# Optimization experiments

Measured on AMD Instinct MI355X. Metric: run time of the kernel, lower is better.

The kernel has to match this reference:

```python
import jax, jax.numpy as jnp
import numpy as np
from jax import lax

B, L = 4, 1024
D_MODEL, D_STATE, D_CONV = 512, 16, 4
D_INNER = 2 * D_MODEL          # expand=2
DT_RANK = D_MODEL // 16        # ceil(512/16)=32
K_EXPERTS = 2                  # num_experts_per_token; only first k experts are used
EPS = 1e-5


def setup_inputs() -> dict:
    key = jax.random.key(0)
    ks = jax.random.split(key, 14)
    def n(k, shape, scale=0.02):
        return jax.random.normal(k, shape, jnp.float32) * scale
    # Mamba S4D-real init for A: A_log = log(1..d_state) broadcast over channels
    A_log = jnp.log(jnp.broadcast_to(jnp.arange(1, D_STATE + 1, dtype=jnp.float32), (D_INNER, D_STATE)))
    return {
        "x": jax.random.normal(ks[0], (B, L, D_MODEL), jnp.float32),
        "in_proj_w": n(ks[1], (2 * D_INNER, D_MODEL)),
        "conv_w": n(ks[2], (D_INNER, 1, D_CONV), 0.1),
        "conv_b": n(ks[3], (D_INNER,), 0.1),
        "x_proj_w": n(ks[4], (DT_RANK + 2 * D_STATE, D_INNER)),
        "dt_proj_w": n(ks[5], (D_INNER, DT_RANK), 0.1),
        "dt_proj_b": n(ks[6], (D_INNER,), 0.1),
        "A_log": A_log,
        "D_skip": jnp.ones((D_INNER,), jnp.float32),
        "out_proj_w": n(ks[7], (D_MODEL, D_INNER)),
        "moe_w1": n(ks[8], (K_EXPERTS, 2 * D_MODEL, D_MODEL)),
        "moe_b1": n(ks[9], (K_EXPERTS, 2 * D_MODEL)),
        "moe_w2": n(ks[10], (K_EXPERTS, D_MODEL, 2 * D_MODEL)),
        "moe_b2": n(ks[11], (K_EXPERTS, D_MODEL)),
    }


def _layernorm(x):
    # fresh nn.LayerNorm each forward: weight=1, bias=0, eps=1e-5
    mu = jnp.mean(x, -1, keepdims=True)
    var = jnp.mean(jnp.square(x - mu), -1, keepdims=True)
    return (x - mu) / jnp.sqrt(var + EPS)


def _mamba(x, in_proj_w, conv_w, conv_b, x_proj_w, dt_proj_w, dt_proj_b, A_log, D_skip, out_proj_w):
    b = x.shape[0]
    xz = x @ in_proj_w.T                               # (b, L, 2*d_inner)
    xc, z = jnp.split(xz, 2, axis=-1)
    # causal depthwise conv1d (torch pads both sides with d_conv-1 then slices [:L])
    conv = lax.conv_general_dilated(
        xc.transpose(0, 2, 1), conv_w, (1,), [(D_CONV - 1, 0)],
        feature_group_count=D_INNER) + conv_b[None, :, None]
    xs = jax.nn.silu(conv).transpose(0, 2, 1)          # (b, L, d_inner)
    dbc = xs @ x_proj_w.T                              # (b, L, dt_rank + 2*d_state)
    dt = dbc[..., :DT_RANK]
    Bm = dbc[..., DT_RANK:DT_RANK + D_STATE]           # (b, L, d_state)
    Cm = dbc[..., DT_RANK + D_STATE:]                  # (b, L, d_state)
    delta = jax.nn.softplus(dt @ dt_proj_w.T + dt_proj_b)  # (b, L, d_inner)
    A = -jnp.exp(A_log)                                # (d_inner, d_state)
    dA = jnp.exp(jnp.einsum('bld,dn->bldn', delta, A))     # (b, L, d_inner, d_state)
    dBx = (delta * xs)[..., None] * Bm[:, :, None, :]       # (b, L, d_inner, d_state)

    def step(h, inp):
        dA_t, dBx_t, C_t = inp
        h = dA_t * h + dBx_t                           # (b, d_inner, d_state)
        y = jnp.einsum('bdn,bn->bd', h, C_t)
        return h, y

    h0 = jnp.zeros((b, D_INNER, D_STATE), x.dtype)
    _, ys = lax.scan(step, h0, (dA.transpose(1, 0, 2, 3), dBx.transpose(1, 0, 2, 3), Cm.transpose(1, 0, 2)))
    y = ys.transpose(1, 0, 2) + xs * D_skip            # (b, L, d_inner)
    y = y * jax.nn.silu(z)
    return y @ out_proj_w.T                            # (b, L, d_model)


def reference(x, in_proj_w, conv_w, conv_b, x_proj_w, dt_proj_w, dt_proj_b,
              A_log, D_skip, out_proj_w, moe_w1, moe_b1, moe_w2, moe_b2):
    skip = x
    h = _layernorm(x)
    h = _mamba(h, in_proj_w, conv_w, conv_b, x_proj_w, dt_proj_w, dt_proj_b, A_log, D_skip, out_proj_w) + h
    h = _layernorm(h)
    # static 'MoE': unweighted average of the first K_EXPERTS dense FFNs
    a = jax.nn.relu(jnp.einsum('bld,ekd->belk', h, moe_w1) + moe_b1[None, :, None, :])
    moe = jnp.einsum('belk,edk->beld', a, moe_w2) + moe_b2[None, :, None, :]
    return jnp.mean(moe, axis=1) + skip
```

## Files before the change

### kernel.cpp

```cpp
#include <hip/hip_runtime.h>
#include <hip/hip_bf16.h>

#define BB 4
#define LL 1024
#define DM 512
#define DI 1024
#define DS 16
#define DTR 32
#define MM (BB*LL)

#define ACT_NONE 0
#define ACT_RELU 1

#define CHUNK 128
#define NCH (LL/CHUNK)
#define NSTATE 65536

typedef __attribute__((ext_vector_type(8))) __bf16 bf16x8;
typedef __attribute__((ext_vector_type(8))) unsigned short us8;
typedef __attribute__((ext_vector_type(4))) float f32x4;

__device__ __forceinline__ unsigned short f2bf(float f) {
  union { float f; unsigned int u; } a; a.f = f;
  unsigned int r = a.u + 0x7fffu + ((a.u >> 16) & 1u);
  return (unsigned short)(r >> 16);
}
__device__ __forceinline__ float b2f(unsigned short u) {
  union { unsigned int i; float f; } a; a.i = (unsigned int)u << 16; return a.f;
}

__device__ __forceinline__ bf16x8 ld_frag(const unsigned short* p) {
  us8 s = *(const us8*)p;
  return __builtin_bit_cast(bf16x8, s);
}

__device__ __forceinline__ void gload16(const void* g, void* l) {
  __builtin_amdgcn_global_load_lds(
      (const __attribute__((address_space(1))) void*)g,
      (__attribute__((address_space(3))) void*)l, 16, 0, 0);
}

__global__ __launch_bounds__(256) void prep_ln_kernel(
    const float* __restrict__ x,
    const float* __restrict__ in_proj_w, const float* __restrict__ x_proj_w,
    const float* __restrict__ out_proj_w,
    const float* __restrict__ moe_w1,    const float* __restrict__ moe_w2,
    const float* __restrict__ moe_b2,
    float* __restrict__ h1, unsigned short* __restrict__ h1b,
    unsigned short* __restrict__ inpb,  unsigned short* __restrict__ xpjb,
    unsigned short* __restrict__ outpb,
    unsigned short* __restrict__ w1b,   unsigned short* __restrict__ w2cb,
    float* __restrict__ b2avg)
{
  __shared__ float red[8];
  int bid = blockIdx.x;
  if (bid < MM) {
    int row = bid;
    const float* p = x + (size_t)row * DM;
    float2 v = ((const float2*)p)[threadIdx.x];
    float s  = v.x + v.y;
    float ss = v.x*v.x + v.y*v.y;
    for (int o = 32; o; o >>= 1) { s += __shfl_down(s, o); ss += __shfl_down(ss, o); }
    int wid = threadIdx.x >> 6, lane = threadIdx.x & 63;
    if (lane == 0) { red[wid] = s; red[4+wid] = ss; }
    __syncthreads();
    s  = red[0]+red[1]+red[2]+red[3];
    ss = red[4]+red[5]+red[6]+red[7];
    float mu = s * (1.f/DM);
    float var = ss * (1.f/DM) - mu*mu;
    float rstd = rsqrtf(var + 1e-5f);
    float2 o2; o2.x = (v.x-mu)*rstd; o2.y = (v.y-mu)*rstd;
    ((float2*)(h1 + (size_t)row*DM))[threadIdx.x] = o2;
    ushort2 u; u.x = f2bf(o2.x); u.y = f2bf(o2.y);
    ((ushort2*)(h1b + (size_t)row*DM))[threadIdx.x] = u;
    return;
  }
  int i = (bid - MM) * 256 + threadIdx.x;
  int i4 = i * 4;
  auto cvt4 = [&](const float* src, unsigned short* dst) {
    float4 v = ((const float4*)src)[i];
    ushort4 o; o.x = f2bf(v.x); o.y = f2bf(v.y); o.z = f2bf(v.z); o.w = f2bf(v.w);
    ((ushort4*)dst)[i] = o;
  };
  if (i4 < 2*DI*DM) cvt4(in_proj_w, inpb);
  if (i4 < 64*DI)   cvt4(x_proj_w, xpjb);
  if (i4 < DM*DI)   cvt4(out_proj_w, outpb);
  if (i4 < 2*(2*DM)*DM) cvt4(moe_w1, w1b);
  if (i4 < DM*2*DI) {
    #pragma unroll
    for (int j = 0; j < 4; ++j) {
      int idx = i4 + j;
      int nrow = idx >> 11;
      int t = idx & (2*DI - 1);
      int e = t >> 10;
      int k = t & (DI - 1);
      w2cb[idx] = f2bf(moe_w2[((size_t)e*DM + nrow)*DI + k]);
    }
  }
  if (i4 < DM) {
    #pragma unroll
    for (int j = 0; j < 4; ++j)
      b2avg[i4+j] = 0.5f * (moe_b2[i4+j] + moe_b2[DM + i4+j]);
  }
}

__global__ __launch_bounds__(256) void ln_kernel(const float* __restrict__ in,
                                                 float* __restrict__ outf,
                                                 unsigned short* __restrict__ outb) {
  int row = blockIdx.x;
  const float* p = in + (size_t)row * DM;
  float2 v = ((const float2*)p)[threadIdx.x];
  float s  = v.x + v.y;
  float ss = v.x*v.x + v.y*v.y;
  for (int o = 32; o; o >>= 1) { s += __shfl_down(s, o); ss += __shfl_down(ss, o); }
  __shared__ float red[8];
  int wid = threadIdx.x >> 6, lane = threadIdx.x & 63;
  if (lane == 0) { red[wid] = s; red[4+wid] = ss; }
  __syncthreads();
  s  = red[0]+red[1]+red[2]+red[3];
  ss = red[4]+red[5]+red[6]+red[7];
  float mu = s * (1.f/DM);
  float var = ss * (1.f/DM) - mu*mu;
  float rstd = rsqrtf(var + 1e-5f);
  float2 o2; o2.x = (v.x-mu)*rstd; o2.y = (v.y-mu)*rstd;
  if (outf) ((float2*)(outf + (size_t)row*DM))[threadIdx.x] = o2;
  if (outb) {
    ushort2 u; u.x = f2bf(o2.x); u.y = f2bf(o2.y);
    ((ushort2*)(outb + (size_t)row*DM))[threadIdx.x] = u;
  }
}

template<int BM, int BN, int BK, int WR, int WC, int FM, int FN, int ACT,
         bool OUTF, bool OUTB>
__global__ __launch_bounds__(256) void gemm_mfma(
    const unsigned short* __restrict__ A, int lda,
    const unsigned short* __restrict__ B, int ldb,
    const float* __restrict__ bias,
    const float* __restrict__ res, int ldres,
    float* __restrict__ Cf, unsigned short* __restrict__ Cb, int ldc,
    int K, float scale, int nbx)
{
  static_assert(WR*WC == 4 && WR*FM*16 == BM && WC*FN*16 == BN, "geom");
  constexpr int ATILE = BM*BK, BTILE = BN*BK;
  constexpr int AL = ATILE/2048, BL = BTILE/2048;
  constexpr bool SWZ = (BK == 64);
  __shared__ unsigned short As[2*ATILE];
  __shared__ unsigned short Bs[2*BTILE];
  const int tid = threadIdx.x;
  const int nwg = gridDim.x;
  const int bid = blockIdx.x;
  const int cpx = nwg >> 3;
  const int wid = ((nwg & 7) == 0) ? ((bid & 7)*cpx + (bid >> 3)) : bid;
  const int bm = (wid / nbx) * BM;
  const int bn = (wid % nbx) * BN;
  const int w = tid >> 6, lane = tid & 63;
  const int wr = w / WC, wc = w % WC;
  const int rl = lane & 15, kg = lane >> 4;

  auto stage = [&](int buf, int k0) {
    #pragma unroll
    for (int it = 0; it < AL; ++it) {
      int o = (it*256 + tid) * 16;
      int os = SWZ ? (o ^ (((o>>7)&7)<<4)) : o;
      int e = os >> 1;
      int r = e / BK, c = e % BK;
      gload16(A + (size_t)(bm + r)*lda + k0 + c, (char*)As + buf*ATILE*2 + o);
    }
    #pragma unroll
    for (int it = 0; it < BL; ++it) {
      int o = (it*256 + tid) * 16;
      int os = SWZ ? (o ^ (((o>>7)&7)<<4)) : o;
      int e = os >> 1;
      int r = e / BK, c = e % BK;
      gload16(B + (size_t)(bn + r)*ldb + k0 + c, (char*)Bs + buf*BTILE*2 + o);
    }
  };

  f32x4 acc[FM][FN];
  #pragma unroll
  for (int m = 0; m < FM; ++m)
    #pragma unroll
    for (int n = 0; n < FN; ++n) { f32x4 z = {0.f,0.f,0.f,0.f}; acc[m][n] = z; }

  auto compute = [&](int buf) {
    #pragma unroll
    for (int kk = 0; kk < BK/32; ++kk) {
      bf16x8 af[FM], bfv[FN];
      #pragma unroll
      for (int m = 0; m < FM; ++m) {
        int byte = ((wr*FM*16 + m*16 + rl)*BK + kk*32 + kg*8) * 2;
        if (SWZ) byte ^= ((byte>>7)&7)<<4;
        af[m] = ld_frag((const unsigned short*)((const char*)As + buf*ATILE*2 + byte));
      }
      #pragma unroll
      for (int n = 0; n < FN; ++n) {
        int byte = ((wc*FN*16 + n*16 + rl)*BK + kk*32 + kg*8) * 2;
        if (SWZ) byte ^= ((byte>>7)&7)<<4;
        bfv[n] = ld_frag((const unsigned short*)((const char*)Bs + buf*BTILE*2 + byte));
      }
      #pragma unroll
      for (int m = 0; m < FM; ++m)
        #pragma unroll
        for (int n = 0; n < FN; ++n)
          acc[m][n] = __builtin_amdgcn_mfma_f32_16x16x32_bf16(af[m], bfv[n], acc[m][n], 0, 0, 0);
    }
  };

  stage(0, 0);
  const int nk = K / BK;
  for (int it = 0; it < nk; ++it) {
    if (it + 1 < nk) {
      stage((it&1)^1, (it+1)*BK);
      asm volatile("s_waitcnt vmcnt(%0)" :: "i"(AL+BL) : "memory");
    } else {
      asm volatile("s_waitcnt vmcnt(0)" ::: "memory");
    }
    __builtin_amdgcn_s_barrier();
    compute(it & 1);
    __builtin_amdgcn_s_barrier();
  }

  #pragma unroll
  for (int m = 0; m < FM; ++m) {
    int row = bm + wr*FM*16 + m*16 + kg*4;
    #pragma unroll
    for (int n = 0; n < FN; ++n) {
      int col = bn + wc*FN*16 + n*16 + rl;
      float bv = bias ? bias[col] : 0.f;
      #pragma unroll
      for (int j = 0; j < 4; ++j) {
        float v = acc[m][n][j] * scale + bv;
        if (ACT == ACT_RELU) v = fmaxf(v, 0.f);
        if (res) v += res[(size_t)(row + j)*ldres + col];
        size_t off = (size_t)(row + j)*ldc + col;
        if (OUTF) Cf[off] = v;
        if (OUTB) Cb[off] = f2bf(v);
      }
    }
  }
}

__global__ __launch_bounds__(256) void conv_silu_kernel(
    const unsigned short* __restrict__ xzb, const float* __restrict__ conv_w,
    const float* __restrict__ conv_b, unsigned short* __restrict__ xsb)
{
  int t = blockIdx.x * 256 + threadIdx.x;
  int d8 = (t & (DI/8 - 1)) * 8;
  int l = (t >> 7) & (LL-1);
  int b = t >> 17;
  size_t base = (size_t)(b*LL) * 2*DI + d8;
  float acc[8];
  #pragma unroll
  for (int j = 0; j < 8; ++j) acc[j] = conv_b[d8+j];
  #pragma unroll
  for (int k = 0; k < 4; ++k) {
    int ll = l - 3 + k;
    if (ll >= 0) {
      us8 v = *(const us8*)(xzb + base + (size_t)ll * 2*DI);
      #pragma unroll
      for (int j = 0; j < 8; ++j)
        acc[j] = fmaf(conv_w[(d8+j)*4 + k], b2f((unsigned short)v[j]), acc[j]);
    }
  }
  us8 o;
  #pragma unroll
  for (int j = 0; j < 8; ++j) {
    float s = acc[j];
    float v = s / (1.f + __expf(-s));
    o[j] = (unsigned short)f2bf(v);
  }
  *(us8*)(xsb + (size_t)((b*LL + l)*DI) + d8) = o;
}

__global__ __launch_bounds__(256) void scan_p1(
    const float* __restrict__ dbc,
    const unsigned short* __restrict__ xsb,
    const float* __restrict__ dtw,
    const float* __restrict__ dtb,
    const float* __restrict__ A_log,
    float* __restrict__ P, float* __restrict__ Q,
    unsigned short* __restrict__ deltab)
{
  int blk = blockIdx.x;
  int c  = blk & (NCH-1);
  int dg = (blk >> 3) & 63;
  int b  = blk >> 9;
  int tid = threadIdx.x;
  int g = tid >> 4, n = tid & 15;
  int d0 = dg*16;
  float Adn2 = -__expf(A_log[(d0+g)*DS + n]) * 1.44269504f;
  __shared__ float s_d[16][68], s_dx[16][68], s_B[16][68];
  __shared__ float s_dt[64][33];
  __shared__ float s_w[16][32];
  __shared__ float s_bs[16];
  {
    int dr = tid >> 5, jc = tid & 31;
    s_w[dr][jc]   = dtw[(d0+dr)*DTR + jc];
    s_w[dr+8][jc] = dtw[(d0+dr+8)*DTR + jc];
    if (tid < 16) s_bs[tid] = dtb[d0 + tid];
  }
  float h = 0.f, S = 0.f;
  int lbase = c*CHUNK;
  for (int l0 = 0; l0 < CHUNK; l0 += 64) {
    {
      int li = tid >> 2, dd = (tid & 3) * 4;
      size_t row = (size_t)b*LL + lbase + l0 + li;
      ushort4 ux = *(const ushort4*)(xsb + row*DI + d0 + dd);
      float4 vB = *(const float4*)(dbc + row*64 + 32 + dd);
      float4 t0 = *(const float4*)(dbc + row*64 + dd);
      float4 t1 = *(const float4*)(dbc + row*64 + 16 + dd);
      s_dx[dd+0][li]=b2f(ux.x); s_dx[dd+1][li]=b2f(ux.y);
      s_dx[dd+2][li]=b2f(ux.z); s_dx[dd+3][li]=b2f(ux.w);
      s_B [dd+0][li]=vB.x; s_B [dd+1][li]=vB.y; s_B [dd+2][li]=vB.z; s_B [dd+3][li]=vB.w;
      *(float4*)&s_dt[li][dd]      = t0;
      *(float4*)&s_dt[li][16 + dd] = t1;
    }
    __syncthreads();
    {
      int l = tid & 63, dq = tid >> 6;
      size_t row = (size_t)b*LL + lbase + l0 + l;
      ushort4 dout;
      #pragma unroll
      for (int k = 0; k < 4; ++k) {
        int d = dq*4 + k;
        float acc = s_bs[d];
        #pragma unroll
        for (int j = 0; j < 32; j += 4) {
          float4 wt  = *(const float4*)&s_w[d][j];
          float4 dt4 = *(const float4*)&s_dt[l][j];
          acc = fmaf(wt.x, dt4.x, acc); acc = fmaf(wt.y, dt4.y, acc);
          acc = fmaf(wt.z, dt4.z, acc); acc = fmaf(wt.w, dt4.w, acc);
        }
        float sp = fmaxf(acc, 0.f) + log1pf(__expf(-fabsf(acc)));
        unsigned short spb = f2bf(sp);
        float spf = b2f(spb);
        ((unsigned short*)&dout)[k] = spb;
        s_d[d][l] = spf;
        s_dx[d][l] *= spf;
      }
      *(ushort4*)(deltab + row*DI + d0 + dq*4) = dout;
    }
    __syncthreads();
    #pragma unroll
    for (int q4 = 0; q4 < 64; q4 += 4) {
      float4 vd  = *(const float4*)&s_d[g][q4];
      float4 vdx = *(const float4*)&s_dx[g][q4];
      float4 vB  = *(const float4*)&s_B[n][q4];
      float dA;
      dA = exp2f(vd.x*Adn2); h = fmaf(dA, h, vdx.x*vB.x); S += vd.x;
      dA = exp2f(vd.y*Adn2); h = fmaf(dA, h, vdx.y*vB.y); S += vd.y;
      dA = exp2f(vd.z*Adn2); h = fmaf(dA, h, vdx.z*vB.z); S += vd.z;
      dA = exp2f(vd.w*Adn2); h = fmaf(dA, h, vdx.w*vB.w); S += vd.w;
    }
    __syncthreads();
  }
  int base = ((b*64 + dg)*256 + g*16 + n) + NSTATE*c;
  P[base] = exp2f(S * Adn2);
  Q[base] = h;
}

__global__ __launch_bounds__(256) void scan_p2(
    const unsigned short* __restrict__ deltab,
    const unsigned short* __restrict__ xsb,
    const unsigned short* __restrict__ xzb,
    const float* __restrict__ dbc,
    const float* __restrict__ A_log,
    const float* __restrict__ D_skip,
    const float* __restrict__ P, const float* __restrict__ Q,
    unsigned short* __restrict__ ymulb)
{
  int blk = blockIdx.x;
  int c  = blk & (NCH-1);
  int dg = (blk >> 3) & 63;
  int b  = blk >> 9;
  int tid = threadIdx.x;
  int g = tid >> 4, n = tid & 15;
  int d0 = dg*16;
  float Adn2 = -__expf(A_log[(d0+g)*DS + n]) * 1.44269504f;
  __shared__ float s_d[16][68], s_dx[16][68], s_B[16][68], s_C[16][68];
  __shared__ float s_z[64][17], s_t[64][17];
  __shared__ float s_yp[16][16][17];
  float h = 0.f;
  {
    int t = (b*64 + dg)*256 + g*16 + n;
    for (int cc = 0; cc < c; ++cc)
      h = fmaf(P[t + NSTATE*cc], h, Q[t + NSTATE*cc]);
  }
  int lbase = c*CHUNK;
  for (int l0 = 0; l0 < CHUNK; l0 += 64) {
    {
      int li = tid >> 2, dd = (tid & 3) * 4;
      size_t row = (size_t)b*LL + lbase + l0 + li;
      ushort4 ud = *(const ushort4*)(deltab + row*DI + d0 + dd);
      ushort4 ux = *(const ushort4*)(xsb    + row*DI + d0 + dd);
      ushort4 uz = *(const ushort4*)(xzb    + row*2*DI + DI + d0 + dd);
      float4 vB = *(const float4*)(dbc   + row*64 + 32 + dd);
      float4 vC = *(const float4*)(dbc   + row*64 + 48 + dd);
      float4 vD = *(const float4*)(D_skip + d0 + dd);
      float dx_ = b2f(ud.x), dy_ = b2f(ud.y), dz_ = b2f(ud.z), dw_ = b2f(ud.w);
      float xx_ = b2f(ux.x), xy_ = b2f(ux.y), xz2 = b2f(ux.z), xw_ = b2f(ux.w);
      float zx_ = b2f(uz.x), zy_ = b2f(uz.y), zz_ = b2f(uz.z), zw_ = b2f(uz.w);
      s_d [dd+0][li]=dx_; s_d [dd+1][li]=dy_; s_d [dd+2][li]=dz_; s_d [dd+3][li]=dw_;
      s_dx[dd+0][li]=dx_*xx_; s_dx[dd+1][li]=dy_*xy_; s_dx[dd+2][li]=dz_*xz2; s_dx[dd+3][li]=dw_*xw_;
      s_B [dd+0][li]=vB.x; s_B [dd+1][li]=vB.y; s_B [dd+2][li]=vB.z; s_B [dd+3][li]=vB.w;
      s_C [dd+0][li]=vC.x; s_C [dd+1][li]=vC.y; s_C [dd+2][li]=vC.z; s_C [dd+3][li]=vC.w;
      float szx = zx_ / (1.f + __expf(-zx_));
      float szy = zy_ / (1.f + __expf(-zy_));
      float szz = zz_ / (1.f + __expf(-zz_));
      float szw = zw_ / (1.f + __expf(-zw_));
      s_z[li][dd+0]=szx; s_z[li][dd+1]=szy; s_z[li][dd+2]=szz; s_z[li][dd+3]=szw;
      s_t[li][dd+0]=xx_*vD.x*szx; s_t[li][dd+1]=xy_*vD.y*szy;
      s_t[li][dd+2]=xz2*vD.z*szz; s_t[li][dd+3]=xw_*vD.w*szw;
    }
    __syncthreads();
    #pragma unroll
    for (int sub = 0; sub < 4; ++sub) {
      #pragma unroll
      for (int q4 = 0; q4 < 16; q4 += 4) {
        int li = sub*16 + q4;
        float4 vd  = *(const float4*)&s_d[g][li];
        float4 vdx = *(const float4*)&s_dx[g][li];
        float4 vB  = *(const float4*)&s_B[n][li];
        float4 vC  = *(const float4*)&s_C[n][li];
        float dA;
        dA = exp2f(vd.x*Adn2); h = fmaf(dA, h, vdx.x*vB.x); s_yp[g][n][q4+0] = h*vC.x;
        dA = exp2f(vd.y*Adn2); h = fmaf(dA, h, vdx.y*vB.y); s_yp[g][n][q4+1] = h*vC.y;
        dA = exp2f(vd.z*Adn2); h = fmaf(dA, h, vdx.z*vB.z); s_yp[g][n][q4+2] = h*vC.z;
        dA = exp2f(vd.w*Adn2); h = fmaf(dA, h, vdx.w*vB.w); s_yp[g][n][q4+3] = h*vC.w;
      }
      __syncthreads();
      {
        int q_r = tid & 15, g_r = tid >> 4;
        float y = 0.f;
        #pragma unroll
        for (int nn = 0; nn < 16; ++nn) y += s_yp[g_r][nn][q_r];
        int lis = sub*16 + q_r;
        float v = y * s_z[lis][g_r] + s_t[lis][g_r];
        ymulb[((size_t)b*LL + lbase + l0 + lis)*DI + d0 + g_r] = f2bf(v);
      }
      __syncthreads();
    }
  }
}

extern "C" void kernel_launch(void* const* d_in, const int* in_sizes, int n_in,
                              void* d_out, int out_size, void* d_ws, size_t ws_size,
                              hipStream_t stream) {
  const float* x         = (const float*)d_in[0];
  const float* in_proj_w = (const float*)d_in[1];
  const float* conv_w    = (const float*)d_in[2];
  const float* conv_b    = (const float*)d_in[3];
  const float* x_proj_w  = (const float*)d_in[4];
  const float* dt_proj_w = (const float*)d_in[5];
  const float* dt_proj_b = (const float*)d_in[6];
  const float* A_log     = (const float*)d_in[7];
  const float* D_skip    = (const float*)d_in[8];
  const float* out_proj_w= (const float*)d_in[9];
  const float* moe_w1    = (const float*)d_in[10];
  const float* moe_b1    = (const float*)d_in[11];
  const float* moe_w2    = (const float*)d_in[12];
  const float* moe_b2    = (const float*)d_in[13];
  float* out = (float*)d_out;

  float* p = (float*)d_ws;
  float* h1    = p; p += 2097152;
  float* h2    = p; p += 2097152;
  float* dbc   = p; p += 262144;
  float* Pbuf  = p; p += 524288;
  float* Qbuf  = p; p += 524288;
  float* b2avg = p; p += 1024;
  unsigned short* h1b    = (unsigned short*)p; p += 1048576;
  unsigned short* xzb    = (unsigned short*)p; p += 4194304;
  unsigned short* xsb    = (unsigned short*)p; p += 2097152;
  unsigned short* deltab = (unsigned short*)p; p += 2097152;
  unsigned short* ymulb  = (unsigned short*)p; p += 2097152;
  unsigned short* h2lnb  = (unsigned short*)p; p += 1048576;
  unsigned short* acatb  = (unsigned short*)p; p += 4194304;
  unsigned short* inpb   = (unsigned short*)p; p += 524288;
  unsigned short* xpjb   = (unsigned short*)p; p += 32768;
  unsigned short* outpb  = (unsigned short*)p; p += 262144;
  unsigned short* w1b    = (unsigned short*)p; p += 524288;
  unsigned short* w2cb   = (unsigned short*)p; p += 524288;

  prep_ln_kernel<<<MM + 1024, 256, 0, stream>>>(x, in_proj_w, x_proj_w, out_proj_w,
                                                moe_w1, moe_w2, moe_b2,
                                                h1, h1b, inpb, xpjb, outpb, w1b, w2cb, b2avg);
  gemm_mfma<128,128,64,2,2,4,4,ACT_NONE,false,true><<<512, 256, 0, stream>>>(
      h1b, DM, inpb, DM, nullptr, nullptr, 0, nullptr, xzb, 2*DI, DM, 1.f, 16);
  conv_silu_kernel<<<(MM*DI/8)/256, 256, 0, stream>>>(xzb, conv_w, conv_b, xsb);
  gemm_mfma<64,64,64,2,2,2,2,ACT_NONE,true,false><<<64, 256, 0, stream>>>(
      xsb, DI, xpjb, DI, nullptr, nullptr, 0, dbc, nullptr, 64, DI, 1.f, 1);
  scan_p1<<<BB*64*NCH, 256, 0, stream>>>(dbc, xsb, dt_proj_w, dt_proj_b, A_log,
                                         Pbuf, Qbuf, deltab);
  scan_p2<<<BB*64*NCH, 256, 0, stream>>>(deltab, xsb, xzb, dbc, A_log, D_skip,
                                         Pbuf, Qbuf, ymulb);
  gemm_mfma<64,64,64,2,2,2,2,ACT_NONE,true,false><<<512, 256, 0, stream>>>(
      ymulb, DI, outpb, DI, nullptr, h1, DM, h2, nullptr, DM, DI, 1.f, 8);
  ln_kernel<<<MM, 256, 0, stream>>>(h2, nullptr, h2lnb);
  gemm_mfma<128,128,64,2,2,4,4,ACT_RELU,false,true><<<512, 256, 0, stream>>>(
      h2lnb, DM, w1b, DM, moe_b1, nullptr, 0, nullptr, acatb, 2*DI, DM, 1.f, 16);
  gemm_mfma<64,64,64,2,2,2,2,ACT_NONE,true,false><<<512, 256, 0, stream>>>(
      acatb, 2*DI, w2cb, 2*DI, b2avg, x, DM, out, nullptr, DM, 2*DI, 0.5f, 8);
}
```

Baseline: 211.0 us.

## Restructure selective scan into per-channel chunked three-phase scan with MFMA dt projection

The dt projection and softplus move out of the scan into an MFMA GEMM with a new softplus epilogue. The x_proj GEMM now also writes a bf16 copy of its output, and a small kernel converts dt_proj_w to bf16 to feed that GEMM. The two-pass scan becomes three kernels: per-chunk local scans with chunk size 32, a stitch kernel that carries state across chunks, and a final pass that computes outputs. In the two chunk passes each thread owns one channel and keeps all 16 states in registers. The aim is to remove the shared-memory-heavy 16x16 thread layout, the cross-state reduction, and the redundant per-block prefix over earlier chunks. The cost is extra launches, larger intermediate state buffers, and dt computed in bf16 precision.

```diff
diff --git a/kernel.cpp b/kernel.cpp
--- a/kernel.cpp
+++ b/kernel.cpp
@@ -11,8 +11,9 @@
 
 #define ACT_NONE 0
 #define ACT_RELU 1
-
-#define CHUNK 128
+#define ACT_SP   2
+
+#define CHUNK 32
 #define NCH (LL/CHUNK)
 #define NSTATE 65536
 
@@ -231,6 +232,7 @@
       for (int j = 0; j < 4; ++j) {
         float v = acc[m][n][j] * scale + bv;
         if (ACT == ACT_RELU) v = fmaxf(v, 0.f);
+        if (ACT == ACT_SP)   v = fmaxf(v, 0.f) + log1pf(__expf(-fabsf(v)));
         if (res) v += res[(size_t)(row + j)*ldres + col];
         size_t off = (size_t)(row + j)*ldc + col;
         if (OUTF) Cf[off] = v;
@@ -272,174 +274,131 @@
   *(us8*)(xsb + (size_t)((b*LL + l)*DI) + d8) = o;
 }
 
-__global__ __launch_bounds__(256) void scan_p1(
+__global__ __launch_bounds__(256) void scan_A(
+    const unsigned short* __restrict__ deltab,
+    const unsigned short* __restrict__ xsb,
     const float* __restrict__ dbc,
-    const unsigned short* __restrict__ xsb,
-    const float* __restrict__ dtw,
-    const float* __restrict__ dtb,
     const float* __restrict__ A_log,
-    float* __restrict__ P, float* __restrict__ Q,
-    unsigned short* __restrict__ deltab)
+    float* __restrict__ S, float* __restrict__ Qb)
 {
   int blk = blockIdx.x;
-  int c  = blk & (NCH-1);
-  int dg = (blk >> 3) & 63;
-  int b  = blk >> 9;
+  int dq = blk & 3;
+  int c  = (blk >> 2) & (NCH-1);
+  int b  = blk >> 7;
   int tid = threadIdx.x;
-  int g = tid >> 4, n = tid & 15;
-  int d0 = dg*16;
-  float Adn2 = -__expf(A_log[(d0+g)*DS + n]) * 1.44269504f;
-  __shared__ float s_d[16][68], s_dx[16][68], s_B[16][68];
-  __shared__ float s_dt[64][33];
-  __shared__ float s_w[16][32];
-  __shared__ float s_bs[16];
-  {
-    int dr = tid >> 5, jc = tid & 31;
-    s_w[dr][jc]   = dtw[(d0+dr)*DTR + jc];
-    s_w[dr+8][jc] = dtw[(d0+dr+8)*DTR + jc];
-    if (tid < 16) s_bs[tid] = dtb[d0 + tid];
-  }
-  float h = 0.f, S = 0.f;
-  int lbase = c*CHUNK;
-  for (int l0 = 0; l0 < CHUNK; l0 += 64) {
-    {
-      int li = tid >> 2, dd = (tid & 3) * 4;
-      size_t row = (size_t)b*LL + lbase + l0 + li;
-      ushort4 ux = *(const ushort4*)(xsb + row*DI + d0 + dd);
-      float4 vB = *(const float4*)(dbc + row*64 + 32 + dd);
-      float4 t0 = *(const float4*)(dbc + row*64 + dd);
-      float4 t1 = *(const float4*)(dbc + row*64 + 16 + dd);
-      s_dx[dd+0][li]=b2f(ux.x); s_dx[dd+1][li]=b2f(ux.y);
-      s_dx[dd+2][li]=b2f(ux.z); s_dx[dd+3][li]=b2f(ux.w);
-      s_B [dd+0][li]=vB.x; s_B [dd+1][li]=vB.y; s_B [dd+2][li]=vB.z; s_B [dd+3][li]=vB.w;
-      *(float4*)&s_dt[li][dd]      = t0;
-      *(float4*)&s_dt[li][16 + dd] = t1;
-    }
-    __syncthreads();
-    {
-      int l = tid & 63, dq = tid >> 6;
-      size_t row = (size_t)b*LL + lbase + l0 + l;
-      ushort4 dout;
-      #pragma unroll
-      for (int k = 0; k < 4; ++k) {
-        int d = dq*4 + k;
-        float acc = s_bs[d];
-        #pragma unroll
-        for (int j = 0; j < 32; j += 4) {
-          float4 wt  = *(const float4*)&s_w[d][j];
-          float4 dt4 = *(const float4*)&s_dt[l][j];
-          acc = fmaf(wt.x, dt4.x, acc); acc = fmaf(wt.y, dt4.y, acc);
-          acc = fmaf(wt.z, dt4.z, acc); acc = fmaf(wt.w, dt4.w, acc);
-        }
-        float sp = fmaxf(acc, 0.f) + log1pf(__expf(-fabsf(acc)));
-        unsigned short spb = f2bf(sp);
-        float spf = b2f(spb);
-        ((unsigned short*)&dout)[k] = spb;
-        s_d[d][l] = spf;
-        s_dx[d][l] *= spf;
-      }
-      *(ushort4*)(deltab + row*DI + d0 + dq*4) = dout;
-    }
-    __syncthreads();
-    #pragma unroll
-    for (int q4 = 0; q4 < 64; q4 += 4) {
-      float4 vd  = *(const float4*)&s_d[g][q4];
-      float4 vdx = *(const float4*)&s_dx[g][q4];
-      float4 vB  = *(const float4*)&s_B[n][q4];
-      float dA;
-      dA = exp2f(vd.x*Adn2); h = fmaf(dA, h, vdx.x*vB.x); S += vd.x;
-      dA = exp2f(vd.y*Adn2); h = fmaf(dA, h, vdx.y*vB.y); S += vd.y;
-      dA = exp2f(vd.z*Adn2); h = fmaf(dA, h, vdx.z*vB.z); S += vd.z;
-      dA = exp2f(vd.w*Adn2); h = fmaf(dA, h, vdx.w*vB.w); S += vd.w;
-    }
-    __syncthreads();
-  }
-  int base = ((b*64 + dg)*256 + g*16 + n) + NSTATE*c;
-  P[base] = exp2f(S * Adn2);
-  Q[base] = h;
-}
-
-__global__ __launch_bounds__(256) void scan_p2(
+  int d = dq*256 + tid;
+  float An[16];
+  #pragma unroll
+  for (int n = 0; n < 16; n += 4) {
+    float4 a = *(const float4*)(A_log + d*DS + n);
+    An[n+0] = -__expf(a.x) * 1.44269504f;
+    An[n+1] = -__expf(a.y) * 1.44269504f;
+    An[n+2] = -__expf(a.z) * 1.44269504f;
+    An[n+3] = -__expf(a.w) * 1.44269504f;
+  }
+  __shared__ float s_B[CHUNK][16];
+  for (int i = tid; i < CHUNK*16; i += 256) {
+    int l = i >> 4, n = i & 15;
+    s_B[l][n] = dbc[((size_t)(b*LL) + c*CHUNK + l)*64 + 32 + n];
+  }
+  __syncthreads();
+  float h[16];
+  #pragma unroll
+  for (int n = 0; n < 16; ++n) h[n] = 0.f;
+  float Ssum = 0.f;
+  size_t rowbase = ((size_t)(b*LL) + c*CHUNK)*DI + d;
+  #pragma unroll 4
+  for (int l = 0; l < CHUNK; ++l) {
+    float delta = b2f(deltab[rowbase + (size_t)l*DI]);
+    float xv    = b2f(xsb   [rowbase + (size_t)l*DI]);
+    float dx = delta * xv;
+    Ssum += delta;
+    #pragma unroll
+    for (int n = 0; n < 16; ++n)
+      h[n] = fmaf(exp2f(delta*An[n]), h[n], dx * s_B[l][n]);
+  }
+  S[c*(BB*DI) + b*DI + d] = Ssum;
+  float* q = Qb + (size_t)c*NSTATE + (size_t)(b*DI + d)*16;
+  #pragma unroll
+  for (int n = 0; n < 16; n += 4) {
+    float4 v; v.x = h[n]; v.y = h[n+1]; v.z = h[n+2]; v.w = h[n+3];
+    *(float4*)(q + n) = v;
+  }
+}
+
+__global__ __launch_bounds__(256) void scan_stitch(
+    const float* __restrict__ S, const float* __restrict__ Qb,
+    const float* __restrict__ A_log, float* __restrict__ H)
+{
+  int t = blockIdx.x * 256 + threadIdx.x;
+  int bd = t >> 4, n = t & 15;
+  int d = bd & (DI-1);
+  float An = -__expf(A_log[d*DS + n]) * 1.44269504f;
+  float h = 0.f;
+  for (int c = 0; c < NCH; ++c) {
+    H[(size_t)c*NSTATE + t] = h;
+    h = fmaf(exp2f(S[c*(BB*DI) + bd]*An), h, Qb[(size_t)c*NSTATE + t]);
+  }
+}
+
+__global__ __launch_bounds__(256) void scan_B(
     const unsigned short* __restrict__ deltab,
     const unsigned short* __restrict__ xsb,
     const unsigned short* __restrict__ xzb,
     const float* __restrict__ dbc,
     const float* __restrict__ A_log,
     const float* __restrict__ D_skip,
-    const float* __restrict__ P, const float* __restrict__ Q,
+    const float* __restrict__ H,
     unsigned short* __restrict__ ymulb)
 {
   int blk = blockIdx.x;
-  int c  = blk & (NCH-1);
-  int dg = (blk >> 3) & 63;
-  int b  = blk >> 9;
+  int dq = blk & 3;
+  int c  = (blk >> 2) & (NCH-1);
+  int b  = blk >> 7;
   int tid = threadIdx.x;
-  int g = tid >> 4, n = tid & 15;
-  int d0 = dg*16;
-  float Adn2 = -__expf(A_log[(d0+g)*DS + n]) * 1.44269504f;
-  __shared__ float s_d[16][68], s_dx[16][68], s_B[16][68], s_C[16][68];
-  __shared__ float s_z[64][17], s_t[64][17];
-  __shared__ float s_yp[16][16][17];
-  float h = 0.f;
-  {
-    int t = (b*64 + dg)*256 + g*16 + n;
-    for (int cc = 0; cc < c; ++cc)
-      h = fmaf(P[t + NSTATE*cc], h, Q[t + NSTATE*cc]);
-  }
-  int lbase = c*CHUNK;
-  for (int l0 = 0; l0 < CHUNK; l0 += 64) {
-    {
-      int li = tid >> 2, dd = (tid & 3) * 4;
-      size_t row = (size_t)b*LL + lbase + l0 + li;
-      ushort4 ud = *(const ushort4*)(deltab + row*DI + d0 + dd);
-      ushort4 ux = *(const ushort4*)(xsb    + row*DI + d0 + dd);
-      ushort4 uz = *(const ushort4*)(xzb    + row*2*DI + DI + d0 + dd);
-      float4 vB = *(const float4*)(dbc   + row*64 + 32 + dd);
-      float4 vC = *(const float4*)(dbc   + row*64 + 48 + dd);
-      float4 vD = *(const float4*)(D_skip + d0 + dd);
-      float dx_ = b2f(ud.x), dy_ = b2f(ud.y), dz_ = b2f(ud.z), dw_ = b2f(ud.w);
-      float xx_ = b2f(ux.x), xy_ = b2f(ux.y), xz2 = b2f(ux.z), xw_ = b2f(ux.w);
-      float zx_ = b2f(uz.x), zy_ = b2f(uz.y), zz_ = b2f(uz.z), zw_ = b2f(uz.w);
-      s_d [dd+0][li]=dx_; s_d [dd+1][li]=dy_; s_d [dd+2][li]=dz_; s_d [dd+3][li]=dw_;
-      s_dx[dd+0][li]=dx_*xx_; s_dx[dd+1][li]=dy_*xy_; s_dx[dd+2][li]=dz_*xz2; s_dx[dd+3][li]=dw_*xw_;
-      s_B [dd+0][li]=vB.x; s_B [dd+1][li]=vB.y; s_B [dd+2][li]=vB.z; s_B [dd+3][li]=vB.w;
-      s_C [dd+0][li]=vC.x; s_C [dd+1][li]=vC.y; s_C [dd+2][li]=vC.z; s_C [dd+3][li]=vC.w;
-      float szx = zx_ / (1.f + __expf(-zx_));
-      float szy = zy_ / (1.f + __expf(-zy_));
-      float szz = zz_ / (1.f + __expf(-zz_));
-      float szw = zw_ / (1.f + __expf(-zw_));
-      s_z[li][dd+0]=szx; s_z[li][dd+1]=szy; s_z[li][dd+2]=szz; s_z[li][dd+3]=szw;
-      s_t[li][dd+0]=xx_*vD.x*szx; s_t[li][dd+1]=xy_*vD.y*szy;
-      s_t[li][dd+2]=xz2*vD.z*szz; s_t[li][dd+3]=xw_*vD.w*szw;
-    }
-    __syncthreads();
-    #pragma unroll
-    for (int sub = 0; sub < 4; ++sub) {
-      #pragma unroll
-      for (int q4 = 0; q4 < 16; q4 += 4) {
-        int li = sub*16 + q4;
-        float4 vd  = *(const float4*)&s_d[g][li];
-        float4 vdx = *(const float4*)&s_dx[g][li];
-        float4 vB  = *(const float4*)&s_B[n][li];
-        float4 vC  = *(const float4*)&s_C[n][li];
-        float dA;
-        dA = exp2f(vd.x*Adn2); h = fmaf(dA, h, vdx.x*vB.x); s_yp[g][n][q4+0] = h*vC.x;
-        dA = exp2f(vd.y*Adn2); h = fmaf(dA, h, vdx.y*vB.y); s_yp[g][n][q4+1] = h*vC.y;
-        dA = exp2f(vd.z*Adn2); h = fmaf(dA, h, vdx.z*vB.z); s_yp[g][n][q4+2] = h*vC.z;
-        dA = exp2f(vd.w*Adn2); h = fmaf(dA, h, vdx.w*vB.w); s_yp[g][n][q4+3] = h*vC.w;
-      }
-      __syncthreads();
-      {
-        int q_r = tid & 15, g_r = tid >> 4;
-        float y = 0.f;
-        #pragma unroll
-        for (int nn = 0; nn < 16; ++nn) y += s_yp[g_r][nn][q_r];
-        int lis = sub*16 + q_r;
-        float v = y * s_z[lis][g_r] + s_t[lis][g_r];
-        ymulb[((size_t)b*LL + lbase + l0 + lis)*DI + d0 + g_r] = f2bf(v);
-      }
-      __syncthreads();
-    }
+  int d = dq*256 + tid;
+  float An[16];
+  #pragma unroll
+  for (int n = 0; n < 16; n += 4) {
+    float4 a = *(const float4*)(A_log + d*DS + n);
+    An[n+0] = -__expf(a.x) * 1.44269504f;
+    An[n+1] = -__expf(a.y) * 1.44269504f;
+    An[n+2] = -__expf(a.z) * 1.44269504f;
+    An[n+3] = -__expf(a.w) * 1.44269504f;
+  }
+  float Dd = D_skip[d];
+  __shared__ float s_B[CHUNK][16], s_C[CHUNK][16];
+  for (int i = tid; i < CHUNK*16; i += 256) {
+    int l = i >> 4, n = i & 15;
+    size_t row = (size_t)(b*LL) + c*CHUNK + l;
+    s_B[l][n] = dbc[row*64 + 32 + n];
+    s_C[l][n] = dbc[row*64 + 48 + n];
+  }
+  __syncthreads();
+  float h[16];
+  const float* hp = H + (size_t)c*NSTATE + (size_t)(b*DI + d)*16;
+  #pragma unroll
+  for (int n = 0; n < 16; n += 4) {
+    float4 v = *(const float4*)(hp + n);
+    h[n] = v.x; h[n+1] = v.y; h[n+2] = v.z; h[n+3] = v.w;
+  }
+  size_t rowbase = ((size_t)(b*LL) + c*CHUNK)*DI + d;
+  size_t zbase   = ((size_t)(b*LL) + c*CHUNK)*2*DI + DI + d;
+  #pragma unroll 4
+  for (int l = 0; l < CHUNK; ++l) {
+    float delta = b2f(deltab[rowbase + (size_t)l*DI]);
+    float xv    = b2f(xsb   [rowbase + (size_t)l*DI]);
+    float zv    = b2f(xzb   [zbase   + (size_t)l*2*DI]);
+    float dx = delta * xv;
+    float y = 0.f;
+    #pragma unroll
+    for (int n = 0; n < 16; ++n) {
+      h[n] = fmaf(exp2f(delta*An[n]), h[n], dx * s_B[l][n]);
+      y = fmaf(h[n], s_C[l][n], y);
+    }
+    float sz = zv / (1.f + __expf(-zv));
+    float v = (y + xv*Dd) * sz;
+    ymulb[rowbase + (size_t)l*DI] = f2bf(v);
   }
 }
 
@@ -466,18 +425,21 @@
   float* h1    = p; p += 2097152;
   float* h2    = p; p += 2097152;
   float* dbc   = p; p += 262144;
-  float* Pbuf  = p; p += 524288;
-  float* Qbuf  = p; p += 524288;
+  float* Sbuf  = p; p += 131072;
+  float* Qbuf  = p; p += 2097152;
+  float* Hbuf  = p; p += 2097152;
   float* b2avg = p; p += 1024;
   unsigned short* h1b    = (unsigned short*)p; p += 1048576;
   unsigned short* xzb    = (unsigned short*)p; p += 4194304;
   unsigned short* xsb    = (unsigned short*)p; p += 2097152;
   unsigned short* deltab = (unsigned short*)p; p += 2097152;
+  unsigned short* dbcb   = (unsigned short*)p; p += 131072;
   unsigned short* ymulb  = (unsigned short*)p; p += 2097152;
   unsigned short* h2lnb  = (unsigned short*)p; p += 1048576;
   unsigned short* acatb  = (unsigned short*)p; p += 4194304;
   unsigned short* inpb   = (unsigned short*)p; p += 524288;
   unsigned short* xpjb   = (unsigned short*)p; p += 32768;
+  unsigned short* dtpb   = (unsigned short*)p; p += 16384;
   unsigned short* outpb  = (unsigned short*)p; p += 262144;
   unsigned short* w1b    = (unsigned short*)p; p += 524288;
   unsigned short* w2cb   = (unsigned short*)p; p += 524288;
@@ -485,15 +447,27 @@
   prep_ln_kernel<<<MM + 1024, 256, 0, stream>>>(x, in_proj_w, x_proj_w, out_proj_w,
                                                 moe_w1, moe_w2, moe_b2,
                                                 h1, h1b, inpb, xpjb, outpb, w1b, w2cb, b2avg);
+  {
+    struct K { static __global__ void f(const float* s, unsigned short* d) {
+      int i = blockIdx.x*256 + threadIdx.x;
+      if (i < 32768/4) {
+        float4 v = ((const float4*)s)[i];
+        ushort4 o; o.x = f2bf(v.x); o.y = f2bf(v.y); o.z = f2bf(v.z); o.w = f2bf(v.w);
+        ((ushort4*)d)[i] = o;
+      }
+    }};
+    K::f<<<32, 256, 0, stream>>>(dt_proj_w, dtpb);
+  }
   gemm_mfma<128,128,64,2,2,4,4,ACT_NONE,false,true><<<512, 256, 0, stream>>>(
       h1b, DM, inpb, DM, nullptr, nullptr, 0, nullptr, xzb, 2*DI, DM, 1.f, 16);
   conv_silu_kernel<<<(MM*DI/8)/256, 256, 0, stream>>>(xzb, conv_w, conv_b, xsb);
-  gemm_mfma<64,64,64,2,2,2,2,ACT_NONE,true,false><<<64, 256, 0, stream>>>(
-      xsb, DI, xpjb, DI, nullptr, nullptr, 0, dbc, nullptr, 64, DI, 1.f, 1);
-  scan_p1<<<BB*64*NCH, 256, 0, stream>>>(dbc, xsb, dt_proj_w, dt_proj_b, A_log,
-                                         Pbuf, Qbuf, deltab);
-  scan_p2<<<BB*64*NCH, 256, 0, stream>>>(deltab, xsb, xzb, dbc, A_log, D_skip,
-                                         Pbuf, Qbuf, ymulb);
+  gemm_mfma<64,64,64,2,2,2,2,ACT_NONE,true,true><<<64, 256, 0, stream>>>(
+      xsb, DI, xpjb, DI, nullptr, nullptr, 0, dbc, dbcb, 64, DI, 1.f, 1);
+  gemm_mfma<128,128,32,2,2,4,4,ACT_SP,false,true><<<256, 256, 0, stream>>>(
+      dbcb, 64, dtpb, DTR, dt_proj_b, nullptr, 0, nullptr, deltab, DI, DTR, 1.f, 8);
+  scan_A<<<BB*NCH*4, 256, 0, stream>>>(deltab, xsb, dbc, A_log, Sbuf, Qbuf);
+  scan_stitch<<<NSTATE/256, 256, 0, stream>>>(Sbuf, Qbuf, A_log, Hbuf);
+  scan_B<<<BB*NCH*4, 256, 0, stream>>>(deltab, xsb, xzb, dbc, A_log, D_skip, Hbuf, ymulb);
   gemm_mfma<64,64,64,2,2,2,2,ACT_NONE,true,false><<<512, 256, 0, stream>>>(
       ymulb, DI, outpb, DI, nullptr, h1, DM, h2, nullptr, DM, DI, 1.f, 8);
   ln_kernel<<<MM, 256, 0, stream>>>(h2, nullptr, h2lnb);
```

Result: slower. 223.1 us (+5.8%).
